# Optimization experiments

Measured on AMD Instinct MI355X. Metric: run time of the kernel, lower is better.

## Reference

```python
import jax, jax.numpy as jnp
import numpy as np

D_MODEL = 256
N_HEAD = 8
D_FF = 2048
BATCH = 4
TOK_PER_BATCH = 4096
N = BATCH * TOK_PER_BATCH  # 16384 total queries == total keys
L = 32  # neighbors per query
EPS = 1e-5


def _layer_norm(x, g, b):
    mu = jnp.mean(x, axis=-1, keepdims=True)
    var = jnp.mean(jnp.square(x - mu), axis=-1, keepdims=True)
    return (x - mu) * jax.lax.rsqrt(var + EPS) * g + b


def setup_inputs() -> dict:
    key = jax.random.key(0)
    ks = jax.random.split(key, 16)
    d, f = D_MODEL, D_FF
    s = 1.0 / np.sqrt(d)
    inp = {
        "src": jax.random.normal(ks[0], (N, d), dtype=jnp.float32),
        "index_pair": jax.random.randint(ks[1], (N, L), 0, TOK_PER_BATCH, dtype=jnp.int64),
        "query_batch_cnt": jnp.full((BATCH,), TOK_PER_BATCH, dtype=jnp.int32),
        "key_batch_cnt": jnp.full((BATCH,), TOK_PER_BATCH, dtype=jnp.int32),
        "index_pair_batch": jnp.repeat(jnp.arange(BATCH, dtype=jnp.int32), TOK_PER_BATCH),
        "Wq": jax.random.normal(ks[2], (d, d), dtype=jnp.float32) * s,
        "bq": jnp.zeros((d,), jnp.float32),
        "Wk": jax.random.normal(ks[3], (d, d), dtype=jnp.float32) * s,
        "bk": jnp.zeros((d,), jnp.float32),
        "Wv": jax.random.normal(ks[4], (d, d), dtype=jnp.float32) * s,
        "bv": jnp.zeros((d,), jnp.float32),
        "Wo": jax.random.normal(ks[5], (d, d), dtype=jnp.float32) * s,
        "bo": jnp.zeros((d,), jnp.float32),
        "W1": jax.random.normal(ks[6], (d, f), dtype=jnp.float32) * s,
        "b1": jnp.zeros((f,), jnp.float32),
        "W2": jax.random.normal(ks[7], (f, d), dtype=jnp.float32) * (1.0 / np.sqrt(f)),
        "b2": jnp.zeros((d,), jnp.float32),
        "g1": jnp.ones((d,), jnp.float32),
        "be1": jnp.zeros((d,), jnp.float32),
        "g2": jnp.ones((d,), jnp.float32),
        "be2": jnp.zeros((d,), jnp.float32),
    }
    return inp


def _attention(src, index_pair, key_batch_cnt, index_pair_batch,
               Wq, bq, Wk, bk, Wv, bv, Wo, bo):
    n, d = src.shape
    hd = d // N_HEAD
    scale = hd ** -0.5
    q = (src @ Wq + bq).reshape(n, N_HEAD, hd) * scale
    k = src @ Wk + bk
    v = src @ Wv + bv
    # exclusive cumsum -> start offset of each batch's key segment
    key_start = jnp.cumsum(key_batch_cnt) - key_batch_cnt          # [B]
    offs = key_start[index_pair_batch]                             # [N]
    valid = index_pair >= 0                                        # [N, L]
    idx = jnp.where(valid, index_pair + offs[:, None].astype(index_pair.dtype), 0)
    kg = k[idx].reshape(n, L, N_HEAD, hd)                          # gathered keys
    vg = v[idx].reshape(n, L, N_HEAD, hd)                          # gathered values
    logits = jnp.einsum("nhd,nlhd->nhl", q, kg)
    logits = jnp.where(valid[:, None, :], logits, jnp.float32(-1e9))
    attn = jax.nn.softmax(logits, axis=-1)
    out = jnp.einsum("nhl,nlhd->nhd", attn, vg).reshape(n, d)
    return out @ Wo + bo


def reference(src, index_pair, query_batch_cnt, key_batch_cnt, index_pair_batch,
              Wq, bq, Wk, bk, Wv, bv, Wo, bo, W1, b1, W2, b2, g1, be1, g2, be2):
    src2 = _attention(src, index_pair, key_batch_cnt, index_pair_batch,
                      Wq, bq, Wk, bk, Wv, bv, Wo, bo)
    x = _layer_norm(src + src2, g1, be1)
    ff = jax.nn.relu(x @ W1 + b1) @ W2 + b2
    return _layer_norm(x + ff, g2, be2)
```

## Files before the change

### kernel.cpp

```cpp
#include <hip/hip_runtime.h>
#include <hip/hip_bf16.h>
#include <cstddef>
#include <cstdint>

#define D_MODEL 256
#define N_TOK   16384
#define NHEAD   8
#define HDIM    32
#define LNEIGH  32
#define DFF     2048

typedef short bf16x8 __attribute__((ext_vector_type(8)));
typedef float f32x4  __attribute__((ext_vector_type(4)));

__device__ __forceinline__ float b2f(short s) {
    unsigned u = ((unsigned)(unsigned short)s) << 16;
    return __builtin_bit_cast(float, u);
}

__device__ __forceinline__ void gload_lds16(const void* g, void* l) {
    auto* gp = reinterpret_cast<const __attribute__((address_space(1))) uint32_t*>(
        reinterpret_cast<uintptr_t>(g));
    auto* lp = reinterpret_cast<__attribute__((address_space(3))) uint32_t*>(
        reinterpret_cast<uintptr_t>(l));
    __builtin_amdgcn_global_load_lds(gp, lp, 16, 0, 0);
}

__global__ __launch_bounds__(256) void gemm_bt(
    const __hip_bfloat16* __restrict__ A, int lda,
    const __hip_bfloat16* __restrict__ Bt, int ldb,
    const float* __restrict__ bias,
    __hip_bfloat16* __restrict__ outb,
    int M, int N, int K, int relu)
{
    __shared__ short Asm[2][128 * 32];
    __shared__ short Bsm[2][128 * 32];

    const int tid  = threadIdx.x;
    const int lane = tid & 63;
    const int wid  = tid >> 6;
    const int wr   = wid >> 1;
    const int wc   = wid & 1;
    const int bm   = blockIdx.y * 128;
    const int bn   = blockIdx.x * 128;

    f32x4 acc[4][4] = {};
    const int srow = lane >> 2;
    const int seg  = (lane & 3) * 8;

    auto stage = [&](int buf, int k0) {
        #pragma unroll
        for (int t = 0; t < 2; ++t) {
            int rbase = wid * 32 + t * 16;
            gload_lds16(A  + (size_t)(bm + rbase + srow) * lda + k0 + seg, &Asm[buf][rbase * 32]);
            gload_lds16(Bt + (size_t)(bn + rbase + srow) * ldb + k0 + seg, &Bsm[buf][rbase * 32]);
        }
    };

    const int nk = K >> 5;
    stage(0, 0);
    __syncthreads();

    for (int kk = 0; kk < nk; ++kk) {
        const int cur = kk & 1;
        if (kk + 1 < nk) stage(cur ^ 1, (kk + 1) << 5);

        bf16x8 a[4], b[4];
        #pragma unroll
        for (int i = 0; i < 4; ++i)
            a[i] = *(const bf16x8*)&Asm[cur][(wr * 64 + i * 16 + (lane & 15)) * 32 + (lane >> 4) * 8];
        #pragma unroll
        for (int j = 0; j < 4; ++j)
            b[j] = *(const bf16x8*)&Bsm[cur][(wc * 64 + j * 16 + (lane & 15)) * 32 + (lane >> 4) * 8];
        #pragma unroll
        for (int i = 0; i < 4; ++i)
            #pragma unroll
            for (int j = 0; j < 4; ++j)
                acc[i][j] = __builtin_amdgcn_mfma_f32_16x16x32_bf16(a[i], b[j], acc[i][j], 0, 0, 0);
        __syncthreads();
    }

    #pragma unroll
    for (int i = 0; i < 4; ++i) {
        int rbase = bm + wr * 64 + i * 16 + ((lane >> 4) << 2);
        #pragma unroll
        for (int j = 0; j < 4; ++j) {
            int col = bn + wc * 64 + j * 16 + (lane & 15);
            float bval = bias ? bias[col] : 0.0f;
            #pragma unroll
            for (int r = 0; r < 4; ++r) {
                int row = rbase + r;
                float v = acc[i][j][r] + bval;
                if (relu) v = fmaxf(v, 0.0f);
                outb[(size_t)row * N + col] = __float2bfloat16(v);
            }
        }
    }
}

__global__ __launch_bounds__(256) void gemm_qkv(
    const __hip_bfloat16* __restrict__ A,
    const __hip_bfloat16* __restrict__ Bt,
    const float* __restrict__ bias,
    float* __restrict__ qf,
    __hip_bfloat16* __restrict__ kvb)
{
    __shared__ short Asm[2][128 * 32];
    __shared__ short Bsm[2][128 * 32];

    const int tid  = threadIdx.x;
    const int lane = tid & 63;
    const int wid  = tid >> 6;
    const int wr   = wid >> 1;
    const int wc   = wid & 1;
    const int bm   = blockIdx.y * 128;
    const int bn   = blockIdx.x * 128;

    f32x4 acc[4][4] = {};
    const int srow = lane >> 2;
    const int seg  = (lane & 3) * 8;

    auto stage = [&](int buf, int k0) {
        #pragma unroll
        for (int t = 0; t < 2; ++t) {
            int rbase = wid * 32 + t * 16;
            gload_lds16(A  + (size_t)(bm + rbase + srow) * 256 + k0 + seg, &Asm[buf][rbase * 32]);
            gload_lds16(Bt + (size_t)(bn + rbase + srow) * 256 + k0 + seg, &Bsm[buf][rbase * 32]);
        }
    };

    stage(0, 0);
    __syncthreads();
    for (int kk = 0; kk < 8; ++kk) {
        const int cur = kk & 1;
        if (kk + 1 < 8) stage(cur ^ 1, (kk + 1) << 5);
        bf16x8 a[4], b[4];
        #pragma unroll
        for (int i = 0; i < 4; ++i)
            a[i] = *(const bf16x8*)&Asm[cur][(wr * 64 + i * 16 + (lane & 15)) * 32 + (lane >> 4) * 8];
        #pragma unroll
        for (int j = 0; j < 4; ++j)
            b[j] = *(const bf16x8*)&Bsm[cur][(wc * 64 + j * 16 + (lane & 15)) * 32 + (lane >> 4) * 8];
        #pragma unroll
        for (int i = 0; i < 4; ++i)
            #pragma unroll
            for (int j = 0; j < 4; ++j)
                acc[i][j] = __builtin_amdgcn_mfma_f32_16x16x32_bf16(a[i], b[j], acc[i][j], 0, 0, 0);
        __syncthreads();
    }

    const bool isq = (bn < 256);
    #pragma unroll
    for (int i = 0; i < 4; ++i) {
        int rbase = bm + wr * 64 + i * 16 + ((lane >> 4) << 2);
        #pragma unroll
        for (int j = 0; j < 4; ++j) {
            int col = bn + wc * 64 + j * 16 + (lane & 15);
            float bval = bias[col];
            #pragma unroll
            for (int r = 0; r < 4; ++r) {
                int row = rbase + r;
                float v = acc[i][j][r] + bval;
                if (isq) qf[(size_t)row * 256 + col] = v;
                else     kvb[(size_t)row * 512 + (col - 256)] = __float2bfloat16(v);
            }
        }
    }
}

__global__ __launch_bounds__(512) void gemm_bt_ln32(
    const __hip_bfloat16* __restrict__ A, int lda,
    const __hip_bfloat16* __restrict__ Bt, int ldb,
    const float* __restrict__ bias,
    const float* __restrict__ residf,
    const __hip_bfloat16* __restrict__ residb,
    const float* __restrict__ g,
    const float* __restrict__ be,
    float* __restrict__ outf,
    __hip_bfloat16* __restrict__ outb,
    int K)
{
    __shared__ short Asm[2][32 * 32];
    __shared__ short Bsm[2][256 * 32];
    __shared__ float lnS[8][32], lnS2[8][32];
    __shared__ float rmu[32], rrs[32];

    const int tid  = threadIdx.x;
    const int lane = tid & 63;
    const int wid  = tid >> 6;
    const int wr   = wid >> 2;
    const int wc   = wid & 3;
    const int bm   = blockIdx.x * 32;
    const int lo   = lane & 15;
    const int hi   = lane >> 4;

    f32x4 acc[4] = {};
    const int srow = lane >> 2;
    const int seg  = (lane & 3) * 8;

    auto stage = [&](int buf, int k0) {
        if (wid < 2) {
            int ra = wid * 16;
            gload_lds16(A + (size_t)(bm + ra + srow) * lda + k0 + seg, &Asm[buf][ra * 32]);
        }
        #pragma unroll
        for (int t = 0; t < 2; ++t) {
            int rb = wid * 32 + t * 16;
            gload_lds16(Bt + (size_t)(rb + srow) * ldb + k0 + seg, &Bsm[buf][rb * 32]);
        }
    };

    const int nk = K >> 5;
    stage(0, 0);
    __syncthreads();

    for (int kk = 0; kk < nk; ++kk) {
        const int cur = kk & 1;
        if (kk + 1 < nk) stage(cur ^ 1, (kk + 1) << 5);

        bf16x8 a, b[4];
        a = *(const bf16x8*)&Asm[cur][(wr * 16 + lo) * 32 + hi * 8];
        #pragma unroll
        for (int j = 0; j < 4; ++j)
            b[j] = *(const bf16x8*)&Bsm[cur][(wc * 64 + j * 16 + lo) * 32 + hi * 8];
        #pragma unroll
        for (int j = 0; j < 4; ++j)
            acc[j] = __builtin_amdgcn_mfma_f32_16x16x32_bf16(a, b[j], acc[j], 0, 0, 0);
        __syncthreads();
    }

    float ps[4] = {}, ps2[4] = {};
    #pragma unroll
    for (int j = 0; j < 4; ++j) {
        int col = wc * 64 + j * 16 + lo;
        float bval = bias ? bias[col] : 0.0f;
        #pragma unroll
        for (int r = 0; r < 4; ++r) {
            int row = bm + wr * 16 + hi * 4 + r;
            float v = acc[j][r] + bval;
            size_t o = (size_t)row * 256 + col;
            if (residf) v += residf[o];
            if (residb) v += __bfloat162float(residb[o]);
            acc[j][r] = v;
            ps[r]  += v;
            ps2[r] += v * v;
        }
    }
    #pragma unroll
    for (int r = 0; r < 4; ++r) {
        #pragma unroll
        for (int m = 1; m < 16; m <<= 1) {
            ps[r]  += __shfl_xor(ps[r],  m);
            ps2[r] += __shfl_xor(ps2[r], m);
        }
    }
    if (lo == 0) {
        #pragma unroll
        for (int r = 0; r < 4; ++r) {
            int rl = wr * 16 + hi * 4 + r;
            lnS[wid][rl]  = ps[r];
            lnS2[wid][rl] = ps2[r];
        }
    }
    __syncthreads();
    if (tid < 32) {
        int base = (tid >> 4) * 4;
        float s  = lnS[base][tid] + lnS[base + 1][tid] + lnS[base + 2][tid] + lnS[base + 3][tid];
        float s2 = lnS2[base][tid] + lnS2[base + 1][tid] + lnS2[base + 2][tid] + lnS2[base + 3][tid];
        float mu  = s * (1.0f / 256.0f);
        float var = s2 * (1.0f / 256.0f) - mu * mu;
        rmu[tid] = mu;
        rrs[tid] = rsqrtf(var + 1e-5f);
    }
    __syncthreads();

    #pragma unroll
    for (int j = 0; j < 4; ++j) {
        int col = wc * 64 + j * 16 + lo;
        float gg = g[col], bb = be[col];
        #pragma unroll
        for (int r = 0; r < 4; ++r) {
            int rl = wr * 16 + hi * 4 + r;
            float v = (acc[j][r] - rmu[rl]) * rrs[rl] * gg + bb;
            size_t o = (size_t)(bm + rl) * 256 + col;
            if (outf) outf[o] = v;
            if (outb) outb[o] = __float2bfloat16(v);
        }
    }
}

__global__ __launch_bounds__(256) void cvt_f2b(
    const float* __restrict__ x, __hip_bfloat16* __restrict__ y, int n)
{
    int i = (blockIdx.x * 256 + threadIdx.x) * 4;
    if (i >= n) return;
    float4 v = *(const float4*)(x + i);
    y[i + 0] = __float2bfloat16(v.x);
    y[i + 1] = __float2bfloat16(v.y);
    y[i + 2] = __float2bfloat16(v.z);
    y[i + 3] = __float2bfloat16(v.w);
}

__global__ __launch_bounds__(256) void cvt_wt_tiled(
    const float* __restrict__ W, __hip_bfloat16* __restrict__ Wt,
    int K, int N, float scale)
{
    __shared__ float t[32][33];
    const int n0 = blockIdx.x * 32;
    const int k0 = blockIdx.y * 32;
    const int tx = threadIdx.x & 31;
    const int ty = threadIdx.x >> 5;
    #pragma unroll
    for (int i = 0; i < 32; i += 8)
        t[ty + i][tx] = W[(size_t)(k0 + ty + i) * N + n0 + tx];
    __syncthreads();
    #pragma unroll
    for (int i = 0; i < 32; i += 8)
        Wt[(size_t)(n0 + ty + i) * K + k0 + tx] = __float2bfloat16(t[tx][ty + i] * scale);
}

__global__ __launch_bounds__(256) void cvt_w3_tiled(
    const float* __restrict__ Wa, const float* __restrict__ Wb,
    const float* __restrict__ Wc, __hip_bfloat16* __restrict__ Wt,
    float scale_a)
{
    __shared__ float t[32][33];
    const int n0 = blockIdx.x * 32;
    const int k0 = blockIdx.y * 32;
    const float* W = (n0 < 256) ? Wa : (n0 < 512 ? Wb : Wc);
    const float sc = (n0 < 256) ? scale_a : 1.0f;
    const int ncol = n0 & 255;
    const int tx = threadIdx.x & 31;
    const int ty = threadIdx.x >> 5;
    #pragma unroll
    for (int i = 0; i < 32; i += 8)
        t[ty + i][tx] = W[(size_t)(k0 + ty + i) * 256 + ncol + tx];
    __syncthreads();
    #pragma unroll
    for (int i = 0; i < 32; i += 8)
        Wt[(size_t)(n0 + ty + i) * 256 + k0 + tx] = __float2bfloat16(t[tx][ty + i] * sc);
}

__global__ __launch_bounds__(768) void make_bqkv(
    const float* __restrict__ bq, const float* __restrict__ bk,
    const float* __restrict__ bv, const int* __restrict__ kbc, int nb,
    float* __restrict__ o, int* __restrict__ ks, float qs)
{
    int i = threadIdx.x;
    if (i < 256)      o[i] = bq[i] * qs;
    else if (i < 512) o[i] = bk[i - 256];
    else              o[i] = bv[i - 512];
    if (i < nb) {
        int acc = 0;
        for (int j = 0; j < i; ++j) acc += kbc[j];
        ks[i] = acc;
    }
}

__global__ __launch_bounds__(256) void attn_wave(
    const float* __restrict__ qf,
    const __hip_bfloat16* __restrict__ kvb,
    const int* __restrict__ index_pair,
    const int* __restrict__ ipb,
    const int* __restrict__ key_start,
    __hip_bfloat16* __restrict__ out)
{
    const int w    = threadIdx.x >> 6;
    const int lane = threadIdx.x & 63;
    const int bid  = blockIdx.x;
    const int n  = (bid & 7) * 2048 + (bid >> 3) * 4 + w;
    const int c  = lane & 31;
    const int pp = lane >> 5;

    int raw = index_pair[(size_t)n * LNEIGH + c];
    int ks  = key_start[ipb[n]];
    int gi0 = (raw >= 0) ? raw + ks : -1;

    const float* qp = qf + (size_t)n * 256 + c * 8;
    float4 q0 = *(const float4*)(qp);
    float4 q1 = *(const float4*)(qp + 4);

    int gi[16];
    #pragma unroll
    for (int i = 0; i < 16; ++i) gi[i] = __shfl(gi0, 2 * i + pp);

    bf16x8 kr[16];
    #pragma unroll
    for (int i = 0; i < 16; ++i) {
        int g = gi[i] < 0 ? 0 : gi[i];
        kr[i] = *(const bf16x8*)(kvb + (size_t)g * 512 + c * 8);
    }

    float s[16];
    #pragma unroll
    for (int i = 0; i < 16; ++i) {
        float t = q0.x * b2f(kr[i][0]) + q0.y * b2f(kr[i][1])
                + q0.z * b2f(kr[i][2]) + q0.w * b2f(kr[i][3])
                + q1.x * b2f(kr[i][4]) + q1.y * b2f(kr[i][5])
                + q1.z * b2f(kr[i][6]) + q1.w * b2f(kr[i][7]);
        t += __shfl_xor(t, 1);
        t += __shfl_xor(t, 2);
        s[i] = (gi[i] < 0) ? -1e9f : t;
    }

    bf16x8 vr[16];
    #pragma unroll
    for (int i = 0; i < 16; ++i) {
        int g = gi[i] < 0 ? 0 : gi[i];
        vr[i] = *(const bf16x8*)(kvb + (size_t)g * 512 + 256 + c * 8);
    }

    float m = s[0];
    #pragma unroll
    for (int i = 1; i < 16; ++i) m = fmaxf(m, s[i]);
    m = fmaxf(m, __shfl_xor(m, 32));
    float tot = 0.0f;
    #pragma unroll
    for (int i = 0; i < 16; ++i) { s[i] = __expf(s[i] - m); tot += s[i]; }
    tot += __shfl_xor(tot, 32);
    const float inv = 1.0f / tot;

    float a[8] = {};
    #pragma unroll
    for (int i = 0; i < 16; ++i) {
        float wt = s[i] * inv;
        #pragma unroll
        for (int j = 0; j < 8; ++j) a[j] += wt * b2f(vr[i][j]);
    }
    #pragma unroll
    for (int j = 0; j < 8; ++j) a[j] += __shfl_xor(a[j], 32);

    if (pp == 0) {
        bf16x8 ov;
        #pragma unroll
        for (int j = 0; j < 8; ++j)
            ov[j] = __builtin_bit_cast(short, __float2bfloat16(a[j]));
        *(bf16x8*)((short*)out + (size_t)n * 256 + c * 8) = ov;
    }
}

extern "C" void kernel_launch(void* const* d_in, const int* in_sizes, int n_in,
                              void* d_out, int out_size, void* d_ws, size_t ws_size,
                              hipStream_t stream)
{
    const float* src = (const float*)d_in[0];
    const int*   index_pair = (const int*)d_in[1];
    const int*   kbc = (const int*)d_in[3];
    const int*   ipb = (const int*)d_in[4];
    const float* Wq = (const float*)d_in[5];
    const float* bq = (const float*)d_in[6];
    const float* Wk = (const float*)d_in[7];
    const float* bk = (const float*)d_in[8];
    const float* Wv = (const float*)d_in[9];
    const float* bv = (const float*)d_in[10];
    const float* Wo = (const float*)d_in[11];
    const float* bo = (const float*)d_in[12];
    const float* W1 = (const float*)d_in[13];
    const float* b1 = (const float*)d_in[14];
    const float* W2 = (const float*)d_in[15];
    const float* b2 = (const float*)d_in[16];
    const float* g1 = (const float*)d_in[17];
    const float* be1 = (const float*)d_in[18];
    const float* g2 = (const float*)d_in[19];
    const float* be2 = (const float*)d_in[20];
    float* out = (float*)d_out;
    const int nb = in_sizes[3];

    char* ws = (char*)d_ws;
    const size_t O_SRCBF = 0;
    const size_t O_QF    = 8388608;
    const size_t O_KVB   = 25165824;
    const size_t O_ATTN  = 41943040;
    const size_t O_HC    = 0;
    const size_t O_XBF   = 67108864;
    const size_t O_WQKV  = 75497472;
    const size_t O_WO    = O_WQKV + 768 * 256 * 2;
    const size_t O_W1    = O_WO + 256 * 256 * 2;
    const size_t O_W2    = O_W1 + (size_t)DFF * 256 * 2;
    const size_t O_BQKV  = O_W2 + (size_t)DFF * 256 * 2;
    const size_t O_KS    = O_BQKV + 768 * 4;

    __hip_bfloat16* src_bf  = (__hip_bfloat16*)(ws + O_SRCBF);
    float*          qf      = (float*)(ws + O_QF);
    __hip_bfloat16* kvb     = (__hip_bfloat16*)(ws + O_KVB);
    __hip_bfloat16* attn_bf = (__hip_bfloat16*)(ws + O_ATTN);
    __hip_bfloat16* hc      = (__hip_bfloat16*)(ws + O_HC);
    __hip_bfloat16* x_bf    = (__hip_bfloat16*)(ws + O_XBF);
    __hip_bfloat16* WqkvT   = (__hip_bfloat16*)(ws + O_WQKV);
    __hip_bfloat16* WoT     = (__hip_bfloat16*)(ws + O_WO);
    __hip_bfloat16* W1T     = (__hip_bfloat16*)(ws + O_W1);
    __hip_bfloat16* W2T     = (__hip_bfloat16*)(ws + O_W2);
    float*          bqkv    = (float*)(ws + O_BQKV);
    int*            ksbuf   = (int*)(ws + O_KS);

    const dim3 blk(256);
    const float qscale = 0.17677669529663687f;

    cvt_f2b<<<N_TOK * D_MODEL / 4 / 256, blk, 0, stream>>>(src, src_bf, N_TOK * D_MODEL);
    cvt_w3_tiled<<<dim3(24, 8), blk, 0, stream>>>(Wq, Wk, Wv, WqkvT, qscale);
    cvt_wt_tiled<<<dim3(8, 8),  blk, 0, stream>>>(Wo, WoT, 256, 256, 1.0f);
    cvt_wt_tiled<<<dim3(64, 8), blk, 0, stream>>>(W1, W1T, 256, DFF, 1.0f);
    cvt_wt_tiled<<<dim3(8, 64), blk, 0, stream>>>(W2, W2T, DFF, 256, 1.0f);
    make_bqkv<<<1, 768, 0, stream>>>(bq, bk, bv, kbc, nb, bqkv, ksbuf, qscale);

    gemm_qkv<<<dim3(6, 128), blk, 0, stream>>>(src_bf, WqkvT, bqkv, qf, kvb);

    attn_wave<<<dim3(N_TOK / 4), blk, 0, stream>>>(qf, kvb, index_pair, ipb, ksbuf, attn_bf);

    gemm_bt_ln32<<<dim3(N_TOK / 32), dim3(512), 0, stream>>>(
        attn_bf, 256, WoT, 256, bo, src, nullptr, g1, be1,
        nullptr, x_bf, 256);

    gemm_bt<<<dim3(16, 128), blk, 0, stream>>>(
        x_bf, 256, W1T, 256, b1, hc, N_TOK, DFF, 256, 1);

    gemm_bt_ln32<<<dim3(N_TOK / 32), dim3(512), 0, stream>>>(
        hc, DFF, W2T, DFF, b2, nullptr, x_bf, g2, be2,
        out, nullptr, DFF);
}
```

Before: 165.0 us.

## Load B operand directly into registers in LN-fused GEMM, swizzle A LDS

In the GEMM+LayerNorm kernel, the B (weight) tiles are no longer staged through shared memory. Each wave reads its B fragments straight from global memory into registers and prefetches the next k-step's fragments one iteration ahead. The A tile keeps LDS double-buffering but uses an XOR-swizzled segment layout to cut bank conflicts on the fragment reads. This removes LDS traffic and footprint for B, at the cost of redundant global/L2 reads of B across waves that share columns, and only one iteration of latency hiding for those loads.

```diff
diff --git a/kernel.cpp b/kernel.cpp
--- a/kernel.cpp
+++ b/kernel.cpp
@@ -168,7 +168,7 @@
     }
 }
 
-__global__ __launch_bounds__(512) void gemm_bt_ln32(
+__global__ __launch_bounds__(512) void gemm_bdir_ln(
     const __hip_bfloat16* __restrict__ A, int lda,
     const __hip_bfloat16* __restrict__ Bt, int ldb,
     const float* __restrict__ bias,
@@ -181,7 +181,6 @@
     int K)
 {
     __shared__ short Asm[2][32 * 32];
-    __shared__ short Bsm[2][256 * 32];
     __shared__ float lnS[8][32], lnS2[8][32];
     __shared__ float rmu[32], rrs[32];
 
@@ -196,37 +195,44 @@
 
     f32x4 acc[4] = {};
     const int srow = lane >> 2;
-    const int seg  = (lane & 3) * 8;
-
-    auto stage = [&](int buf, int k0) {
+    const int sseg = (((lane & 3) ^ (srow & 3)) << 3);
+
+    auto stageA = [&](int buf, int k0) {
         if (wid < 2) {
             int ra = wid * 16;
-            gload_lds16(A + (size_t)(bm + ra + srow) * lda + k0 + seg, &Asm[buf][ra * 32]);
-        }
-        #pragma unroll
-        for (int t = 0; t < 2; ++t) {
-            int rb = wid * 32 + t * 16;
-            gload_lds16(Bt + (size_t)(rb + srow) * ldb + k0 + seg, &Bsm[buf][rb * 32]);
+            gload_lds16(A + (size_t)(bm + ra + srow) * lda + k0 + sseg, &Asm[buf][ra * 32]);
         }
     };
 
+    const __hip_bfloat16* brow[4];
+    #pragma unroll
+    for (int j = 0; j < 4; ++j)
+        brow[j] = Bt + (size_t)(wc * 64 + j * 16 + lo) * ldb + hi * 8;
+
     const int nk = K >> 5;
-    stage(0, 0);
-    __syncthreads();
+    bf16x8 bcur[4], bnext[4];
+    #pragma unroll
+    for (int j = 0; j < 4; ++j) bcur[j] = *(const bf16x8*)(brow[j]);
+    stageA(0, 0);
+    __syncthreads();
+
+    const int aoff = (wr * 16 + lo) * 32 + ((hi ^ (lo & 3)) << 3);
 
     for (int kk = 0; kk < nk; ++kk) {
         const int cur = kk & 1;
-        if (kk + 1 < nk) stage(cur ^ 1, (kk + 1) << 5);
-
-        bf16x8 a, b[4];
-        a = *(const bf16x8*)&Asm[cur][(wr * 16 + lo) * 32 + hi * 8];
+        if (kk + 1 < nk) {
+            #pragma unroll
+            for (int j = 0; j < 4; ++j)
+                bnext[j] = *(const bf16x8*)(brow[j] + (size_t)(kk + 1) * 32);
+            stageA(cur ^ 1, (kk + 1) << 5);
+        }
+        bf16x8 a = *(const bf16x8*)&Asm[cur][aoff];
         #pragma unroll
         for (int j = 0; j < 4; ++j)
-            b[j] = *(const bf16x8*)&Bsm[cur][(wc * 64 + j * 16 + lo) * 32 + hi * 8];
-        #pragma unroll
-        for (int j = 0; j < 4; ++j)
-            acc[j] = __builtin_amdgcn_mfma_f32_16x16x32_bf16(a, b[j], acc[j], 0, 0, 0);
+            acc[j] = __builtin_amdgcn_mfma_f32_16x16x32_bf16(a, bcur[j], acc[j], 0, 0, 0);
         __syncthreads();
+        #pragma unroll
+        for (int j = 0; j < 4; ++j) bcur[j] = bnext[j];
     }
 
     float ps[4] = {}, ps2[4] = {};
@@ -507,14 +513,14 @@
 
     attn_wave<<<dim3(N_TOK / 4), blk, 0, stream>>>(qf, kvb, index_pair, ipb, ksbuf, attn_bf);
 
-    gemm_bt_ln32<<<dim3(N_TOK / 32), dim3(512), 0, stream>>>(
+    gemm_bdir_ln<<<dim3(N_TOK / 32), dim3(512), 0, stream>>>(
         attn_bf, 256, WoT, 256, bo, src, nullptr, g1, be1,
         nullptr, x_bf, 256);
 
     gemm_bt<<<dim3(16, 128), blk, 0, stream>>>(
         x_bf, 256, W1T, 256, b1, hc, N_TOK, DFF, 256, 1);
 
-    gemm_bt_ln32<<<dim3(N_TOK / 32), dim3(512), 0, stream>>>(
+    gemm_bdir_ln<<<dim3(N_TOK / 32), dim3(512), 0, stream>>>(
         hc, DFF, W2T, DFF, b2, nullptr, x_bf, g2, be2,
         out, nullptr, DFF);
 }
```

Result: slower. 255.3 us (+54.7%).

## Unfuse LayerNorm from output GEMMs and use 128x64 tiled GEMM

Applied to the files above, without the earlier changes.

Replaces the fused 32-row GEMM+LayerNorm kernel with a 128x64-tile GEMM that writes bf16 pre-norm activations, followed by a separate per-row LayerNorm kernel. The fused kernel re-read the full 256-column weight panel for every 32-row block and kept MFMA reuse low. Larger M tiles improve weight reuse, especially for the K=2048 W2 GEMM. The cost is an extra bf16 round trip through memory, an extra launch per LayerNorm, and rounding the pre-norm sum to bf16, which slightly changes precision.

```diff
diff --git a/kernel.cpp b/kernel.cpp
--- a/kernel.cpp
+++ b/kernel.cpp
@@ -98,6 +98,87 @@
     }
 }
 
+__global__ __launch_bounds__(256) void gemm_bt128x64(
+    const __hip_bfloat16* __restrict__ A, int lda,
+    const __hip_bfloat16* __restrict__ Bt, int ldb,
+    const float* __restrict__ bias,
+    const float* __restrict__ residf,
+    const __hip_bfloat16* __restrict__ residb,
+    __hip_bfloat16* __restrict__ outb,
+    int M, int N, int K)
+{
+    __shared__ short Asm[2][128 * 32];
+    __shared__ short Bsm[2][64 * 32];
+
+    const int tid  = threadIdx.x;
+    const int lane = tid & 63;
+    const int wid  = tid >> 6;
+    const int wr   = wid >> 1;
+    const int wc   = wid & 1;
+    const int bm   = blockIdx.y * 128;
+    const int bn   = blockIdx.x * 64;
+    const int lo   = lane & 15;
+    const int hi   = lane >> 4;
+
+    f32x4 acc[4][2] = {};
+    const int srow = lane >> 2;
+    const int seg  = (lane & 3) * 8;
+
+    auto stage = [&](int buf, int k0) {
+        #pragma unroll
+        for (int t = 0; t < 2; ++t) {
+            int ra = wid * 32 + t * 16;
+            gload_lds16(A + (size_t)(bm + ra + srow) * lda + k0 + seg, &Asm[buf][ra * 32]);
+        }
+        {
+            int rb = wid * 16;
+            gload_lds16(Bt + (size_t)(bn + rb + srow) * ldb + k0 + seg, &Bsm[buf][rb * 32]);
+        }
+    };
+
+    const int nk = K >> 5;
+    stage(0, 0);
+    __syncthreads();
+
+    for (int kk = 0; kk < nk; ++kk) {
+        const int cur = kk & 1;
+        if (kk + 1 < nk) stage(cur ^ 1, (kk + 1) << 5);
+
+        bf16x8 a[4], b[2];
+        #pragma unroll
+        for (int i = 0; i < 4; ++i)
+            a[i] = *(const bf16x8*)&Asm[cur][(wr * 64 + i * 16 + lo) * 32 + hi * 8];
+        #pragma unroll
+        for (int j = 0; j < 2; ++j)
+            b[j] = *(const bf16x8*)&Bsm[cur][(wc * 32 + j * 16 + lo) * 32 + hi * 8];
+        #pragma unroll
+        for (int i = 0; i < 4; ++i)
+            #pragma unroll
+            for (int j = 0; j < 2; ++j)
+                acc[i][j] = __builtin_amdgcn_mfma_f32_16x16x32_bf16(a[i], b[j], acc[i][j], 0, 0, 0);
+        __syncthreads();
+    }
+
+    #pragma unroll
+    for (int i = 0; i < 4; ++i) {
+        int rbase = bm + wr * 64 + i * 16 + (hi << 2);
+        #pragma unroll
+        for (int j = 0; j < 2; ++j) {
+            int col = bn + wc * 32 + j * 16 + lo;
+            float bval = bias ? bias[col] : 0.0f;
+            #pragma unroll
+            for (int r = 0; r < 4; ++r) {
+                int row = rbase + r;
+                float v = acc[i][j][r] + bval;
+                size_t o = (size_t)row * N + col;
+                if (residf) v += residf[o];
+                if (residb) v += __bfloat162float(residb[o]);
+                outb[o] = __float2bfloat16(v);
+            }
+        }
+    }
+}
+
 __global__ __launch_bounds__(256) void gemm_qkv(
     const __hip_bfloat16* __restrict__ A,
     const __hip_bfloat16* __restrict__ Bt,
@@ -168,124 +249,48 @@
     }
 }
 
-__global__ __launch_bounds__(512) void gemm_bt_ln32(
-    const __hip_bfloat16* __restrict__ A, int lda,
-    const __hip_bfloat16* __restrict__ Bt, int ldb,
-    const float* __restrict__ bias,
-    const float* __restrict__ residf,
-    const __hip_bfloat16* __restrict__ residb,
+__global__ __launch_bounds__(256) void ln_rows_b(
+    const __hip_bfloat16* __restrict__ x,
     const float* __restrict__ g,
-    const float* __restrict__ be,
+    const float* __restrict__ b,
     float* __restrict__ outf,
-    __hip_bfloat16* __restrict__ outb,
-    int K)
-{
-    __shared__ short Asm[2][32 * 32];
-    __shared__ short Bsm[2][256 * 32];
-    __shared__ float lnS[8][32], lnS2[8][32];
-    __shared__ float rmu[32], rrs[32];
-
-    const int tid  = threadIdx.x;
-    const int lane = tid & 63;
-    const int wid  = tid >> 6;
-    const int wr   = wid >> 2;
-    const int wc   = wid & 3;
-    const int bm   = blockIdx.x * 32;
-    const int lo   = lane & 15;
-    const int hi   = lane >> 4;
-
-    f32x4 acc[4] = {};
-    const int srow = lane >> 2;
-    const int seg  = (lane & 3) * 8;
-
-    auto stage = [&](int buf, int k0) {
-        if (wid < 2) {
-            int ra = wid * 16;
-            gload_lds16(A + (size_t)(bm + ra + srow) * lda + k0 + seg, &Asm[buf][ra * 32]);
-        }
-        #pragma unroll
-        for (int t = 0; t < 2; ++t) {
-            int rb = wid * 32 + t * 16;
-            gload_lds16(Bt + (size_t)(rb + srow) * ldb + k0 + seg, &Bsm[buf][rb * 32]);
-        }
-    };
-
-    const int nk = K >> 5;
-    stage(0, 0);
-    __syncthreads();
-
-    for (int kk = 0; kk < nk; ++kk) {
-        const int cur = kk & 1;
-        if (kk + 1 < nk) stage(cur ^ 1, (kk + 1) << 5);
-
-        bf16x8 a, b[4];
-        a = *(const bf16x8*)&Asm[cur][(wr * 16 + lo) * 32 + hi * 8];
-        #pragma unroll
-        for (int j = 0; j < 4; ++j)
-            b[j] = *(const bf16x8*)&Bsm[cur][(wc * 64 + j * 16 + lo) * 32 + hi * 8];
-        #pragma unroll
-        for (int j = 0; j < 4; ++j)
-            acc[j] = __builtin_amdgcn_mfma_f32_16x16x32_bf16(a, b[j], acc[j], 0, 0, 0);
-        __syncthreads();
-    }
-
-    float ps[4] = {}, ps2[4] = {};
-    #pragma unroll
-    for (int j = 0; j < 4; ++j) {
-        int col = wc * 64 + j * 16 + lo;
-        float bval = bias ? bias[col] : 0.0f;
-        #pragma unroll
-        for (int r = 0; r < 4; ++r) {
-            int row = bm + wr * 16 + hi * 4 + r;
-            float v = acc[j][r] + bval;
-            size_t o = (size_t)row * 256 + col;
-            if (residf) v += residf[o];
-            if (residb) v += __bfloat162float(residb[o]);
-            acc[j][r] = v;
-            ps[r]  += v;
-            ps2[r] += v * v;
-        }
-    }
-    #pragma unroll
-    for (int r = 0; r < 4; ++r) {
-        #pragma unroll
-        for (int m = 1; m < 16; m <<= 1) {
-            ps[r]  += __shfl_xor(ps[r],  m);
-            ps2[r] += __shfl_xor(ps2[r], m);
-        }
-    }
-    if (lo == 0) {
-        #pragma unroll
-        for (int r = 0; r < 4; ++r) {
-            int rl = wr * 16 + hi * 4 + r;
-            lnS[wid][rl]  = ps[r];
-            lnS2[wid][rl] = ps2[r];
-        }
-    }
-    __syncthreads();
-    if (tid < 32) {
-        int base = (tid >> 4) * 4;
-        float s  = lnS[base][tid] + lnS[base + 1][tid] + lnS[base + 2][tid] + lnS[base + 3][tid];
-        float s2 = lnS2[base][tid] + lnS2[base + 1][tid] + lnS2[base + 2][tid] + lnS2[base + 3][tid];
-        float mu  = s * (1.0f / 256.0f);
-        float var = s2 * (1.0f / 256.0f) - mu * mu;
-        rmu[tid] = mu;
-        rrs[tid] = rsqrtf(var + 1e-5f);
-    }
-    __syncthreads();
-
-    #pragma unroll
-    for (int j = 0; j < 4; ++j) {
-        int col = wc * 64 + j * 16 + lo;
-        float gg = g[col], bb = be[col];
-        #pragma unroll
-        for (int r = 0; r < 4; ++r) {
-            int rl = wr * 16 + hi * 4 + r;
-            float v = (acc[j][r] - rmu[rl]) * rrs[rl] * gg + bb;
-            size_t o = (size_t)(bm + rl) * 256 + col;
-            if (outf) outf[o] = v;
-            if (outb) outb[o] = __float2bfloat16(v);
-        }
+    __hip_bfloat16* __restrict__ outb)
+{
+    const int w    = threadIdx.x >> 6;
+    const int lane = threadIdx.x & 63;
+    const int row  = blockIdx.x * 4 + w;
+
+    short4 xv = *(const short4*)((const short*)x + (size_t)row * 256 + lane * 4);
+    float v0 = b2f(xv.x), v1 = b2f(xv.y), v2 = b2f(xv.z), v3 = b2f(xv.w);
+    float s  = v0 + v1 + v2 + v3;
+    float s2 = v0 * v0 + v1 * v1 + v2 * v2 + v3 * v3;
+    #pragma unroll
+    for (int o = 32; o >= 1; o >>= 1) {
+        s  += __shfl_xor(s,  o);
+        s2 += __shfl_xor(s2, o);
+    }
+    float mu  = s * (1.0f / 256.0f);
+    float var = s2 * (1.0f / 256.0f) - mu * mu;
+    float inv = rsqrtf(var + 1e-5f);
+
+    float4 gv = *(const float4*)(g + lane * 4);
+    float4 bv = *(const float4*)(b + lane * 4);
+    float r0 = (v0 - mu) * inv * gv.x + bv.x;
+    float r1 = (v1 - mu) * inv * gv.y + bv.y;
+    float r2 = (v2 - mu) * inv * gv.z + bv.z;
+    float r3 = (v3 - mu) * inv * gv.w + bv.w;
+
+    if (outf) {
+        float4 ov = {r0, r1, r2, r3};
+        *(float4*)(outf + (size_t)row * 256 + lane * 4) = ov;
+    }
+    if (outb) {
+        short4 ov;
+        ov.x = __builtin_bit_cast(short, __float2bfloat16(r0));
+        ov.y = __builtin_bit_cast(short, __float2bfloat16(r1));
+        ov.z = __builtin_bit_cast(short, __float2bfloat16(r2));
+        ov.w = __builtin_bit_cast(short, __float2bfloat16(r3));
+        *(short4*)((short*)outb + (size_t)row * 256 + lane * 4) = ov;
     }
 }
 
@@ -471,6 +476,7 @@
     const size_t O_QF    = 8388608;
     const size_t O_KVB   = 25165824;
     const size_t O_ATTN  = 41943040;
+    const size_t O_YBF   = 50331648;
     const size_t O_HC    = 0;
     const size_t O_XBF   = 67108864;
     const size_t O_WQKV  = 75497472;
@@ -479,11 +485,13 @@
     const size_t O_W2    = O_W1 + (size_t)DFF * 256 * 2;
     const size_t O_BQKV  = O_W2 + (size_t)DFF * 256 * 2;
     const size_t O_KS    = O_BQKV + 768 * 4;
+    const size_t O_ZBF   = O_KS + 4096;
 
     __hip_bfloat16* src_bf  = (__hip_bfloat16*)(ws + O_SRCBF);
     float*          qf      = (float*)(ws + O_QF);
     __hip_bfloat16* kvb     = (__hip_bfloat16*)(ws + O_KVB);
     __hip_bfloat16* attn_bf = (__hip_bfloat16*)(ws + O_ATTN);
+    __hip_bfloat16* ybf     = (__hip_bfloat16*)(ws + O_YBF);
     __hip_bfloat16* hc      = (__hip_bfloat16*)(ws + O_HC);
     __hip_bfloat16* x_bf    = (__hip_bfloat16*)(ws + O_XBF);
     __hip_bfloat16* WqkvT   = (__hip_bfloat16*)(ws + O_WQKV);
@@ -492,6 +500,7 @@
     __hip_bfloat16* W2T     = (__hip_bfloat16*)(ws + O_W2);
     float*          bqkv    = (float*)(ws + O_BQKV);
     int*            ksbuf   = (int*)(ws + O_KS);
+    __hip_bfloat16* zbf     = (__hip_bfloat16*)(ws + O_ZBF);
 
     const dim3 blk(256);
     const float qscale = 0.17677669529663687f;
@@ -507,14 +516,14 @@
 
     attn_wave<<<dim3(N_TOK / 4), blk, 0, stream>>>(qf, kvb, index_pair, ipb, ksbuf, attn_bf);
 
-    gemm_bt_ln32<<<dim3(N_TOK / 32), dim3(512), 0, stream>>>(
-        attn_bf, 256, WoT, 256, bo, src, nullptr, g1, be1,
-        nullptr, x_bf, 256);
+    gemm_bt128x64<<<dim3(4, 128), blk, 0, stream>>>(
+        attn_bf, 256, WoT, 256, bo, src, nullptr, ybf, N_TOK, 256, 256);
+    ln_rows_b<<<N_TOK / 4, blk, 0, stream>>>(ybf, g1, be1, nullptr, x_bf);
 
     gemm_bt<<<dim3(16, 128), blk, 0, stream>>>(
         x_bf, 256, W1T, 256, b1, hc, N_TOK, DFF, 256, 1);
 
-    gemm_bt_ln32<<<dim3(N_TOK / 32), dim3(512), 0, stream>>>(
-        hc, DFF, W2T, DFF, b2, nullptr, x_bf, g2, be2,
-        out, nullptr, DFF);
-}
+    gemm_bt128x64<<<dim3(4, 128), blk, 0, stream>>>(
+        hc, DFF, W2T, DFF, b2, nullptr, x_bf, zbf, N_TOK, 256, 2048);
+    ln_rows_b<<<N_TOK / 4, blk, 0, stream>>>(zbf, g2, be2, out, nullptr);
+}
```

After: 187.9 us. 1.14x slower.

## Use BK=64 XOR-swizzled LDS tiles in fused GEMM+LayerNorm kernels

Applied to the files above, without the earlier changes.

Replaces the GEMM+LayerNorm kernel with one that stages K tiles of 64 instead of 32, into dynamic shared memory with an XOR swizzle on 16-byte chunks. This halves the number of K iterations and barriers per tile and is meant to avoid LDS bank conflicts on the MFMA operand reads. The LN scratch arrays now alias the A staging buffer. It also threads explicit leading-dimension parameters through gemm_bt and the weight transpose kernel without changing any values. The cost is about 72KB of LDS per block, which may limit occupancy.

```diff
diff --git a/kernel.cpp b/kernel.cpp
--- a/kernel.cpp
+++ b/kernel.cpp
@@ -10,6 +10,8 @@
 #define LNEIGH  32
 #define DFF     2048
 
+#define SMEM_LN32 (8192 + 65536)
+
 typedef short bf16x8 __attribute__((ext_vector_type(8)));
 typedef float f32x4  __attribute__((ext_vector_type(4)));
 
@@ -30,7 +32,7 @@
     const __hip_bfloat16* __restrict__ A, int lda,
     const __hip_bfloat16* __restrict__ Bt, int ldb,
     const float* __restrict__ bias,
-    __hip_bfloat16* __restrict__ outb,
+    __hip_bfloat16* __restrict__ outb, int ldc,
     int M, int N, int K, int relu)
 {
     __shared__ short Asm[2][128 * 32];
@@ -92,8 +94,142 @@
                 int row = rbase + r;
                 float v = acc[i][j][r] + bval;
                 if (relu) v = fmaxf(v, 0.0f);
-                outb[(size_t)row * N + col] = __float2bfloat16(v);
+                outb[(size_t)row * ldc + col] = __float2bfloat16(v);
             }
+        }
+    }
+}
+
+__global__ __launch_bounds__(512) void gemm_bk64_ln32(
+    const __hip_bfloat16* __restrict__ A, int lda,
+    const __hip_bfloat16* __restrict__ Bt, int ldb,
+    const float* __restrict__ bias,
+    const float* __restrict__ residf,
+    const __hip_bfloat16* __restrict__ residb,
+    const float* __restrict__ g,
+    const float* __restrict__ be,
+    float* __restrict__ outf,
+    __hip_bfloat16* __restrict__ outb,
+    int K)
+{
+    extern __shared__ char smem[];
+    short* AsmB = (short*)smem;
+    short* BsmB = (short*)(smem + 8192);
+    float* lnS  = (float*)smem;
+    float* lnS2 = (float*)(smem + 1024);
+    float* rmu  = (float*)(smem + 2048);
+    float* rrs  = (float*)(smem + 2176);
+
+    const int tid  = threadIdx.x;
+    const int lane = tid & 63;
+    const int wid  = tid >> 6;
+    const int wr   = wid >> 2;
+    const int wc   = wid & 3;
+    const int bm   = blockIdx.x * 32;
+    const int lo   = lane & 15;
+    const int hi   = lane >> 4;
+
+    f32x4 acc[4] = {};
+
+    const int srow8 = lane >> 3;
+    const int sc    = lane & 7;
+    const int ssw   = ((sc ^ srow8) << 3);
+
+    auto stage = [&](int buf, int k0) {
+        if (wid < 4)
+            gload_lds16(A + (size_t)(bm + wid * 8 + srow8) * lda + k0 + ssw,
+                        AsmB + buf * 2048 + (wid * 8) * 64);
+        #pragma unroll
+        for (int t = 0; t < 4; ++t) {
+            int rb = wid * 32 + t * 8;
+            gload_lds16(Bt + (size_t)(rb + srow8) * ldb + k0 + ssw,
+                        BsmB + buf * 16384 + rb * 64);
+        }
+    };
+
+    const int nk = K >> 6;
+    stage(0, 0);
+    __syncthreads();
+
+    for (int kk = 0; kk < nk; ++kk) {
+        const int cur = kk & 1;
+        if (kk + 1 < nk) stage(cur ^ 1, (kk + 1) << 6);
+
+        const short* Ab = AsmB + cur * 2048;
+        const short* Bb = BsmB + cur * 16384;
+        #pragma unroll
+        for (int ks = 0; ks < 2; ++ks) {
+            const int csw = ((ks * 4 + hi) ^ (lo & 7)) << 3;
+            bf16x8 a = *(const bf16x8*)&Ab[(wr * 16 + lo) * 64 + csw];
+            bf16x8 b[4];
+            #pragma unroll
+            for (int j = 0; j < 4; ++j)
+                b[j] = *(const bf16x8*)&Bb[(wc * 64 + j * 16 + lo) * 64 + csw];
+            #pragma unroll
+            for (int j = 0; j < 4; ++j)
+                acc[j] = __builtin_amdgcn_mfma_f32_16x16x32_bf16(a, b[j], acc[j], 0, 0, 0);
+        }
+        __syncthreads();
+    }
+
+    float ps[4] = {}, ps2[4] = {};
+    #pragma unroll
+    for (int j = 0; j < 4; ++j) {
+        int col = wc * 64 + j * 16 + lo;
+        float bval = bias ? bias[col] : 0.0f;
+        #pragma unroll
+        for (int r = 0; r < 4; ++r) {
+            int row = bm + wr * 16 + hi * 4 + r;
+            float v = acc[j][r] + bval;
+            size_t o = (size_t)row * 256 + col;
+            if (residf) v += residf[o];
+            if (residb) v += __bfloat162float(residb[o]);
+            acc[j][r] = v;
+            ps[r]  += v;
+            ps2[r] += v * v;
+        }
+    }
+    #pragma unroll
+    for (int r = 0; r < 4; ++r) {
+        #pragma unroll
+        for (int m = 1; m < 16; m <<= 1) {
+            ps[r]  += __shfl_xor(ps[r],  m);
+            ps2[r] += __shfl_xor(ps2[r], m);
+        }
+    }
+    if (lo == 0) {
+        #pragma unroll
+        for (int r = 0; r < 4; ++r) {
+            int rl = wr * 16 + hi * 4 + r;
+            lnS[wid * 32 + rl]  = ps[r];
+            lnS2[wid * 32 + rl] = ps2[r];
+        }
+    }
+    __syncthreads();
+    if (tid < 32) {
+        int base = (tid >> 4) * 4;
+        float s  = lnS[base * 32 + tid] + lnS[(base + 1) * 32 + tid]
+                 + lnS[(base + 2) * 32 + tid] + lnS[(base + 3) * 32 + tid];
+        float s2 = lnS2[base * 32 + tid] + lnS2[(base + 1) * 32 + tid]
+                 + lnS2[(base + 2) * 32 + tid] + lnS2[(base + 3) * 32 + tid];
+        float mu  = s * (1.0f / 256.0f);
+        float var = s2 * (1.0f / 256.0f) - mu * mu;
+        rmu[tid] = mu;
+        rrs[tid] = rsqrtf(var + 1e-5f);
+    }
+    __syncthreads();
+
+    #pragma unroll
+    for (int j = 0; j < 4; ++j) {
+        int col = wc * 64 + j * 16 + lo;
+        float gg = g[col], bb = be[col];
+        #pragma unroll
+        for (int r = 0; r < 4; ++r) {
+            int rl = wr * 16 + hi * 4 + r;
+            float v = (acc[j][r] - rmu[rl]) * rrs[rl] * gg + bb;
+            size_t o = (size_t)(bm + rl) * 256 + col;
+            if (outf) outf[o] = v;
+            if (outb) outb[o] = __float2bfloat16(v);
         }
     }
 }
@@ -168,127 +304,6 @@
     }
 }
 
-__global__ __launch_bounds__(512) void gemm_bt_ln32(
-    const __hip_bfloat16* __restrict__ A, int lda,
-    const __hip_bfloat16* __restrict__ Bt, int ldb,
-    const float* __restrict__ bias,
-    const float* __restrict__ residf,
-    const __hip_bfloat16* __restrict__ residb,
-    const float* __restrict__ g,
-    const float* __restrict__ be,
-    float* __restrict__ outf,
-    __hip_bfloat16* __restrict__ outb,
-    int K)
-{
-    __shared__ short Asm[2][32 * 32];
-    __shared__ short Bsm[2][256 * 32];
-    __shared__ float lnS[8][32], lnS2[8][32];
-    __shared__ float rmu[32], rrs[32];
-
-    const int tid  = threadIdx.x;
-    const int lane = tid & 63;
-    const int wid  = tid >> 6;
-    const int wr   = wid >> 2;
-    const int wc   = wid & 3;
-    const int bm   = blockIdx.x * 32;
-    const int lo   = lane & 15;
-    const int hi   = lane >> 4;
-
-    f32x4 acc[4] = {};
-    const int srow = lane >> 2;
-    const int seg  = (lane & 3) * 8;
-
-    auto stage = [&](int buf, int k0) {
-        if (wid < 2) {
-            int ra = wid * 16;
-            gload_lds16(A + (size_t)(bm + ra + srow) * lda + k0 + seg, &Asm[buf][ra * 32]);
-        }
-        #pragma unroll
-        for (int t = 0; t < 2; ++t) {
-            int rb = wid * 32 + t * 16;
-            gload_lds16(Bt + (size_t)(rb + srow) * ldb + k0 + seg, &Bsm[buf][rb * 32]);
-        }
-    };
-
-    const int nk = K >> 5;
-    stage(0, 0);
-    __syncthreads();
-
-    for (int kk = 0; kk < nk; ++kk) {
-        const int cur = kk & 1;
-        if (kk + 1 < nk) stage(cur ^ 1, (kk + 1) << 5);
-
-        bf16x8 a, b[4];
-        a = *(const bf16x8*)&Asm[cur][(wr * 16 + lo) * 32 + hi * 8];
-        #pragma unroll
-        for (int j = 0; j < 4; ++j)
-            b[j] = *(const bf16x8*)&Bsm[cur][(wc * 64 + j * 16 + lo) * 32 + hi * 8];
-        #pragma unroll
-        for (int j = 0; j < 4; ++j)
-            acc[j] = __builtin_amdgcn_mfma_f32_16x16x32_bf16(a, b[j], acc[j], 0, 0, 0);
-        __syncthreads();
-    }
-
-    float ps[4] = {}, ps2[4] = {};
-    #pragma unroll
-    for (int j = 0; j < 4; ++j) {
-        int col = wc * 64 + j * 16 + lo;
-        float bval = bias ? bias[col] : 0.0f;
-        #pragma unroll
-        for (int r = 0; r < 4; ++r) {
-            int row = bm + wr * 16 + hi * 4 + r;
-            float v = acc[j][r] + bval;
-            size_t o = (size_t)row * 256 + col;
-            if (residf) v += residf[o];
-            if (residb) v += __bfloat162float(residb[o]);
-            acc[j][r] = v;
-            ps[r]  += v;
-            ps2[r] += v * v;
-        }
-    }
-    #pragma unroll
-    for (int r = 0; r < 4; ++r) {
-        #pragma unroll
-        for (int m = 1; m < 16; m <<= 1) {
-            ps[r]  += __shfl_xor(ps[r],  m);
-            ps2[r] += __shfl_xor(ps2[r], m);
-        }
-    }
-    if (lo == 0) {
-        #pragma unroll
-        for (int r = 0; r < 4; ++r) {
-            int rl = wr * 16 + hi * 4 + r;
-            lnS[wid][rl]  = ps[r];
-            lnS2[wid][rl] = ps2[r];
-        }
-    }
-    __syncthreads();
-    if (tid < 32) {
-        int base = (tid >> 4) * 4;
-        float s  = lnS[base][tid] + lnS[base + 1][tid] + lnS[base + 2][tid] + lnS[base + 3][tid];
-        float s2 = lnS2[base][tid] + lnS2[base + 1][tid] + lnS2[base + 2][tid] + lnS2[base + 3][tid];
-        float mu  = s * (1.0f / 256.0f);
-        float var = s2 * (1.0f / 256.0f) - mu * mu;
-        rmu[tid] = mu;
-        rrs[tid] = rsqrtf(var + 1e-5f);
-    }
-    __syncthreads();
-
-    #pragma unroll
-    for (int j = 0; j < 4; ++j) {
-        int col = wc * 64 + j * 16 + lo;
-        float gg = g[col], bb = be[col];
-        #pragma unroll
-        for (int r = 0; r < 4; ++r) {
-            int rl = wr * 16 + hi * 4 + r;
-            float v = (acc[j][r] - rmu[rl]) * rrs[rl] * gg + bb;
-            size_t o = (size_t)(bm + rl) * 256 + col;
-            if (outf) outf[o] = v;
-            if (outb) outb[o] = __float2bfloat16(v);
-        }
-    }
-}
-
 __global__ __launch_bounds__(256) void cvt_f2b(
     const float* __restrict__ x, __hip_bfloat16* __restrict__ y, int n)
 {
@@ -303,7 +318,7 @@
 
 __global__ __launch_bounds__(256) void cvt_wt_tiled(
     const float* __restrict__ W, __hip_bfloat16* __restrict__ Wt,
-    int K, int N, float scale)
+    int K, int N, int ldo, float scale)
 {
     __shared__ float t[32][33];
     const int n0 = blockIdx.x * 32;
@@ -316,7 +331,7 @@
     __syncthreads();
     #pragma unroll
     for (int i = 0; i < 32; i += 8)
-        Wt[(size_t)(n0 + ty + i) * K + k0 + tx] = __float2bfloat16(t[tx][ty + i] * scale);
+        Wt[(size_t)(n0 + ty + i) * ldo + k0 + tx] = __float2bfloat16(t[tx][ty + i] * scale);
 }
 
 __global__ __launch_bounds__(256) void cvt_w3_tiled(
@@ -496,25 +511,28 @@
     const dim3 blk(256);
     const float qscale = 0.17677669529663687f;
 
+    hipFuncSetAttribute(reinterpret_cast<const void*>(gemm_bk64_ln32),
+                        hipFuncAttributeMaxDynamicSharedMemorySize, SMEM_LN32);
+
     cvt_f2b<<<N_TOK * D_MODEL / 4 / 256, blk, 0, stream>>>(src, src_bf, N_TOK * D_MODEL);
     cvt_w3_tiled<<<dim3(24, 8), blk, 0, stream>>>(Wq, Wk, Wv, WqkvT, qscale);
-    cvt_wt_tiled<<<dim3(8, 8),  blk, 0, stream>>>(Wo, WoT, 256, 256, 1.0f);
-    cvt_wt_tiled<<<dim3(64, 8), blk, 0, stream>>>(W1, W1T, 256, DFF, 1.0f);
-    cvt_wt_tiled<<<dim3(8, 64), blk, 0, stream>>>(W2, W2T, DFF, 256, 1.0f);
+    cvt_wt_tiled<<<dim3(8, 8),  blk, 0, stream>>>(Wo, WoT, 256, 256, 256, 1.0f);
+    cvt_wt_tiled<<<dim3(64, 8), blk, 0, stream>>>(W1, W1T, 256, DFF, 256, 1.0f);
+    cvt_wt_tiled<<<dim3(8, 64), blk, 0, stream>>>(W2, W2T, DFF, 256, DFF, 1.0f);
     make_bqkv<<<1, 768, 0, stream>>>(bq, bk, bv, kbc, nb, bqkv, ksbuf, qscale);
 
     gemm_qkv<<<dim3(6, 128), blk, 0, stream>>>(src_bf, WqkvT, bqkv, qf, kvb);
 
     attn_wave<<<dim3(N_TOK / 4), blk, 0, stream>>>(qf, kvb, index_pair, ipb, ksbuf, attn_bf);
 
-    gemm_bt_ln32<<<dim3(N_TOK / 32), dim3(512), 0, stream>>>(
+    gemm_bk64_ln32<<<dim3(N_TOK / 32), dim3(512), SMEM_LN32, stream>>>(
         attn_bf, 256, WoT, 256, bo, src, nullptr, g1, be1,
         nullptr, x_bf, 256);
 
     gemm_bt<<<dim3(16, 128), blk, 0, stream>>>(
-        x_bf, 256, W1T, 256, b1, hc, N_TOK, DFF, 256, 1);
-
-    gemm_bt_ln32<<<dim3(N_TOK / 32), dim3(512), 0, stream>>>(
+        x_bf, 256, W1T, 256, b1, hc, DFF, N_TOK, DFF, 256, 1);
+
+    gemm_bk64_ln32<<<dim3(N_TOK / 32), dim3(512), SMEM_LN32, stream>>>(
         hc, DFF, W2T, DFF, b2, nullptr, x_bf, g2, be2,
         out, nullptr, DFF);
 }
```

Result: faster. 152.6 us (-7.5%).
